# Performance work log

Hardware: AMD Instinct MI355X
Metric: run time of the kernel (lower is better)

## Reference

```python
import jax, jax.numpy as jnp
import numpy as np

K = 4096          # in_features
N = 11008         # out_features
GROUP = 128       # scale group size along K
PACK = 16
BATCH, SEQ = 2, 4096


def setup_inputs() -> dict:
    key = jax.random.key(0)
    k1, k2, k3, k4 = jax.random.split(key, 4)
    x = jax.random.normal(k1, (BATCH, SEQ, K), dtype=jnp.float16)
    # valid ternary codes in {0,1,2} encoding w = code - 1 in {-1,0,+1}
    codes = jax.random.randint(k2, (K, N), 0, 3, dtype=jnp.int32)
    codes = codes.reshape(K // PACK, PACK, N)
    shifts = (2 * jnp.arange(PACK, dtype=jnp.int32))[None, :, None]
    packed_weight = jnp.sum(codes << shifts, axis=1).astype(jnp.int32)  # (K//16, N)
    scales = (jax.random.uniform(k3, (K // GROUP, N), dtype=jnp.float32) * 0.1 + 0.01).astype(jnp.float16)
    bias = (jax.random.normal(k4, (N,), dtype=jnp.float32) * 0.01).astype(jnp.float16)
    return {"x": x, "packed_weight": packed_weight, "scales": scales, "bias": bias}


def _dequant(packed_weight, scales):
    # unpack 16 two-bit codes per int32 along K
    shifts = (2 * jnp.arange(PACK, dtype=jnp.int32))[None, :, None]
    codes = (packed_weight[:, None, :] >> shifts) & 3        # (K//16, 16, N)
    Kp = packed_weight.shape[0] * PACK
    Nn = packed_weight.shape[1]
    w = (codes.astype(jnp.float16) - jnp.float16(1.0)).reshape(Kp, Nn)  # ternary {-1,0,1}
    scale_full = jnp.repeat(scales, GROUP, axis=0)            # (K, N) group-wise gamma
    return w * scale_full


def reference(x, packed_weight, scales, bias):
    Kp = packed_weight.shape[0] * PACK
    Nn = packed_weight.shape[1]
    w = _dequant(packed_weight, scales)                       # (K, N) fp16
    x2 = x.reshape(-1, Kp).astype(jnp.float16)                # (M, K)
    out = jnp.dot(x2, w, preferred_element_type=jnp.float32).astype(jnp.float16)
    out = out + bias
    return out.reshape(*x.shape[:-1], Nn)
```

## Files before the change

kernel.cpp:

```cpp
#include <hip/hip_runtime.h>
#include <stdint.h>

#define K_DIM 4096
#define N_DIM 11008
#define M_DIM 8192
#define BM 128
#define BN 128
#define BK 32
#define ASTRIDE 32
#define BSTRIDE 40
#define NSLAB (K_DIM / BK)

typedef _Float16 half8  __attribute__((ext_vector_type(8)));
typedef _Float16 half2v __attribute__((ext_vector_type(2)));
typedef float    floatx4 __attribute__((ext_vector_type(4)));

__global__ __launch_bounds__(256, 2) void ternary_gemm(
    const float* __restrict__ x,
    const int*   __restrict__ pw,
    const float* __restrict__ scales,
    const float* __restrict__ bias,
    float*       __restrict__ out)
{
    __shared__ __align__(16) _Float16 lds_a[BM * ASTRIDE];
    __shared__ __align__(16) _Float16 lds_b[BN * BSTRIDE];

    const int tid  = threadIdx.x;
    const int lane = tid & 63;
    const int wave = tid >> 6;

    const int n0 = blockIdx.x * BN;
    const int m0 = blockIdx.y * BM;

    const int wm = (wave & 1) * 64;
    const int wn = (wave >> 1) * 64;

    const int nb  = tid & 127;
    const int kpi = tid >> 7;
    const int*   pwp = pw + (size_t)kpi * N_DIM + n0 + nb;
    const float* scp = scales + n0 + nb;
    _Float16* bl = lds_b + nb * BSTRIDE + kpi * 16;

    floatx4 acc[4][4];
    #pragma unroll
    for (int i = 0; i < 4; ++i)
        #pragma unroll
        for (int j = 0; j < 4; ++j)
            acc[i][j] = floatx4{0.f, 0.f, 0.f, 0.f};

    const int lr = lane & 15;
    const int qk = (lane >> 4) * 8;

    for (int slab = 0; slab < NSLAB; ++slab) {
        const int k0 = slab * BK;

        #pragma unroll
        for (int i = 0; i < 4; ++i) {
            const int idx = tid + i * 256;
            const int row = idx >> 3;
            const int kq  = (idx & 7) * 4;
            float4 v4 = *(const float4*)(x + (size_t)(m0 + row) * K_DIM + k0 + kq);
            half2v h0; h0[0] = (_Float16)v4.x; h0[1] = (_Float16)v4.y;
            half2v h1; h1[0] = (_Float16)v4.z; h1[1] = (_Float16)v4.w;
            *(uint2*)(lds_a + row * ASTRIDE + kq) =
                make_uint2(__builtin_bit_cast(uint32_t, h0),
                           __builtin_bit_cast(uint32_t, h1));
        }

        uint32_t v  = (uint32_t)pwp[(size_t)slab * 2 * N_DIM];
        _Float16 sh = (_Float16)scp[(size_t)(slab >> 2) * N_DIM];
        uint32_t sbits = (uint32_t)__builtin_bit_cast(unsigned short, sh);
        uint32_t tmpl = sbits | (((sbits >> 8) ^ 0x80u) << 24);

        uint32_t q[8];
        #pragma unroll
        for (int j = 0; j < 8; ++j) {
            uint32_t t4 = (v >> (4 * j)) & 0xFu;
            uint32_t sp = (t4 | (t4 << 14)) & 0x00030003u;
            uint32_t sel = ((sp & 0x00010001u) << 1) | ((0x00030003u - sp) << 8);
            q[j] = __builtin_amdgcn_perm(tmpl, tmpl, sel);
        }
        *(uint4*)(bl)     = make_uint4(q[0], q[1], q[2], q[3]);
        *(uint4*)(bl + 8) = make_uint4(q[4], q[5], q[6], q[7]);

        __syncthreads();

        half8 af[4], bfr[4];
        #pragma unroll
        for (int t = 0; t < 4; ++t) {
            af[t]  = *(const half8*)&lds_a[(wm + t * 16 + lr) * ASTRIDE + qk];
            bfr[t] = *(const half8*)&lds_b[(wn + t * 16 + lr) * BSTRIDE + qk];
        }
        #pragma unroll
        for (int mt = 0; mt < 4; ++mt)
            #pragma unroll
            for (int nt = 0; nt < 4; ++nt)
                acc[mt][nt] = __builtin_amdgcn_mfma_f32_16x16x32_f16(
                    af[mt], bfr[nt], acc[mt][nt], 0, 0, 0);

        __syncthreads();
    }

    float bv[4];
    #pragma unroll
    for (int nt = 0; nt < 4; ++nt) bv[nt] = bias[n0 + wn + nt * 16 + lr];

    const int rbase = (lane >> 4) * 4;
    #pragma unroll
    for (int mt = 0; mt < 4; ++mt) {
        #pragma unroll
        for (int nt = 0; nt < 4; ++nt) {
            const int col = n0 + wn + nt * 16 + lr;
            float* op = out + (size_t)(m0 + wm + mt * 16 + rbase) * N_DIM + col;
            floatx4 a = acc[mt][nt];
            #pragma unroll
            for (int r = 0; r < 4; ++r)
                op[(size_t)r * N_DIM] = a[r] + bv[nt];
        }
    }
}

extern "C" void kernel_launch(void* const* d_in, const int* in_sizes, int n_in,
                              void* d_out, int out_size, void* d_ws, size_t ws_size,
                              hipStream_t stream) {
    const float* x  = (const float*)d_in[0];
    const int*   pw = (const int*)d_in[1];
    const float* sc = (const float*)d_in[2];
    const float* bs = (const float*)d_in[3];
    float* out = (float*)d_out;

    dim3 grid(N_DIM / BN, M_DIM / BM);
    ternary_gemm<<<grid, 256, 0, stream>>>(x, pw, sc, bs, out);
}
```

Measured before the change: 1.263 ms.

## Split into x conversion, weight dequant prepass, and async-LDS fp16 GEMM

```diff
diff --git a/kernel.cpp b/kernel.cpp
--- a/kernel.cpp
+++ b/kernel.cpp
@@ -7,23 +7,68 @@
 #define BM 128
 #define BN 128
 #define BK 32
-#define ASTRIDE 32
-#define BSTRIDE 40
 #define NSLAB (K_DIM / BK)
 
-typedef _Float16 half8  __attribute__((ext_vector_type(8)));
-typedef _Float16 half2v __attribute__((ext_vector_type(2)));
+typedef _Float16 half8   __attribute__((ext_vector_type(8)));
+typedef _Float16 half2v  __attribute__((ext_vector_type(2)));
 typedef float    floatx4 __attribute__((ext_vector_type(4)));
 
-__global__ __launch_bounds__(256, 2) void ternary_gemm(
-    const float* __restrict__ x,
-    const int*   __restrict__ pw,
-    const float* __restrict__ scales,
-    const float* __restrict__ bias,
-    float*       __restrict__ out)
-{
-    __shared__ __align__(16) _Float16 lds_a[BM * ASTRIDE];
-    __shared__ __align__(16) _Float16 lds_b[BN * BSTRIDE];
+#define WS_X16_BYTES  ((size_t)M_DIM * K_DIM * 2)
+#define WS_W16_BYTES  ((size_t)N_DIM * K_DIM * 2)
+#define WS_NEEDED     (WS_X16_BYTES + WS_W16_BYTES)
+
+__device__ __forceinline__ void async_load16(const void* g, void* l) {
+    __builtin_amdgcn_global_load_lds(
+        (const __attribute__((address_space(1))) void*)g,
+        (__attribute__((address_space(3))) void*)l,
+        16, 0, 0);
+}
+
+__global__ __launch_bounds__(256) void convert_x(
+    const float* __restrict__ x, _Float16* __restrict__ x16)
+{
+    const size_t i = ((size_t)blockIdx.x * 256 + threadIdx.x) * 8;
+    float4 a = *(const float4*)(x + i);
+    float4 b = *(const float4*)(x + i + 4);
+    half8 h;
+    h[0] = (_Float16)a.x; h[1] = (_Float16)a.y; h[2] = (_Float16)a.z; h[3] = (_Float16)a.w;
+    h[4] = (_Float16)b.x; h[5] = (_Float16)b.y; h[6] = (_Float16)b.z; h[7] = (_Float16)b.w;
+    *(half8*)(x16 + i) = h;
+}
+
+__global__ __launch_bounds__(256) void dequant_w(
+    const int* __restrict__ pw, const float* __restrict__ scales,
+    _Float16* __restrict__ w16t)
+{
+    const int kp = (int)(blockIdx.x * 16) + (int)(threadIdx.x & 15);
+    const int n  = (int)(blockIdx.y * 16) + (int)(threadIdx.x >> 4);
+
+    uint32_t v  = (uint32_t)pw[(size_t)kp * N_DIM + n];
+    _Float16 sh = (_Float16)scales[(size_t)(kp >> 3) * N_DIM + n];
+    uint32_t sbits = (uint32_t)__builtin_bit_cast(unsigned short, sh);
+    uint32_t tmpl  = sbits | (((sbits >> 8) ^ 0x80u) << 24);
+
+    uint32_t q[8];
+    #pragma unroll
+    for (int j = 0; j < 8; ++j) {
+        uint32_t t4 = (v >> (4 * j)) & 0xFu;
+        uint32_t sp = (t4 | (t4 << 14)) & 0x00030003u;
+        uint32_t sel = ((sp & 0x00010001u) << 1) | ((0x00030003u - sp) << 8);
+        q[j] = __builtin_amdgcn_perm(tmpl, tmpl, sel);
+    }
+    _Float16* dst = w16t + (size_t)n * K_DIM + (size_t)kp * 16;
+    *(uint4*)(dst)     = make_uint4(q[0], q[1], q[2], q[3]);
+    *(uint4*)(dst + 8) = make_uint4(q[4], q[5], q[6], q[7]);
+}
+
+__global__ __launch_bounds__(256, 2) void gemm_f16(
+    const _Float16* __restrict__ x16,
+    const _Float16* __restrict__ w16t,
+    const float*    __restrict__ bias,
+    float*          __restrict__ out)
+{
+    __shared__ __align__(16) _Float16 lds_a[BM * BK];
+    __shared__ __align__(16) _Float16 lds_b[BN * BK];
 
     const int tid  = threadIdx.x;
     const int lane = tid & 63;
@@ -32,6 +77,87 @@
     const int n0 = blockIdx.x * BN;
     const int m0 = blockIdx.y * BM;
 
+    const int wm = (wave & 1) * 64;
+    const int wn = (wave >> 1) * 64;
+
+    const int sr = tid >> 2;
+    const int sk = (tid & 3) * 8;
+    const _Float16* ag0 = x16  + (size_t)(m0 + sr) * K_DIM + sk;
+    const _Float16* ag1 = ag0 + (size_t)64 * K_DIM;
+    const _Float16* bg0 = w16t + (size_t)(n0 + sr) * K_DIM + sk;
+    const _Float16* bg1 = bg0 + (size_t)64 * K_DIM;
+    _Float16* al = lds_a + tid * 8;
+    _Float16* blp = lds_b + tid * 8;
+
+    floatx4 acc[4][4];
+    #pragma unroll
+    for (int i = 0; i < 4; ++i)
+        #pragma unroll
+        for (int j = 0; j < 4; ++j)
+            acc[i][j] = floatx4{0.f, 0.f, 0.f, 0.f};
+
+    const int lr = lane & 15;
+    const int qk = (lane >> 4) * 8;
+
+    for (int slab = 0; slab < NSLAB; ++slab) {
+        const size_t ko = (size_t)slab * BK;
+        async_load16(ag0 + ko, al);
+        async_load16(ag1 + ko, al + 2048);
+        async_load16(bg0 + ko, blp);
+        async_load16(bg1 + ko, blp + 2048);
+
+        __syncthreads();
+
+        half8 af[4], bf[4];
+        #pragma unroll
+        for (int t = 0; t < 4; ++t) {
+            af[t] = *(const half8*)&lds_a[(wm + t * 16 + lr) * BK + qk];
+            bf[t] = *(const half8*)&lds_b[(wn + t * 16 + lr) * BK + qk];
+        }
+        #pragma unroll
+        for (int mt = 0; mt < 4; ++mt)
+            #pragma unroll
+            for (int nt = 0; nt < 4; ++nt)
+                acc[mt][nt] = __builtin_amdgcn_mfma_f32_16x16x32_f16(
+                    af[mt], bf[nt], acc[mt][nt], 0, 0, 0);
+
+        __syncthreads();
+    }
+
+    float bv[4];
+    #pragma unroll
+    for (int nt = 0; nt < 4; ++nt) bv[nt] = bias[n0 + wn + nt * 16 + lr];
+
+    const int rbase = (lane >> 4) * 4;
+    #pragma unroll
+    for (int mt = 0; mt < 4; ++mt) {
+        #pragma unroll
+        for (int nt = 0; nt < 4; ++nt) {
+            const int col = n0 + wn + nt * 16 + lr;
+            float* op = out + (size_t)(m0 + wm + mt * 16 + rbase) * N_DIM + col;
+            floatx4 a = acc[mt][nt];
+            #pragma unroll
+            for (int r = 0; r < 4; ++r)
+                op[(size_t)r * N_DIM] = a[r] + bv[nt];
+        }
+    }
+}
+
+#define ASTRIDE 40
+#define BSTRIDE 40
+__global__ __launch_bounds__(256, 2) void ternary_gemm_fused(
+    const float* __restrict__ x, const int* __restrict__ pw,
+    const float* __restrict__ scales, const float* __restrict__ bias,
+    float* __restrict__ out)
+{
+    __shared__ __align__(16) _Float16 lds_a[BM * ASTRIDE];
+    __shared__ __align__(16) _Float16 lds_b[BN * BSTRIDE];
+
+    const int tid  = threadIdx.x;
+    const int lane = tid & 63;
+    const int wave = tid >> 6;
+    const int n0 = blockIdx.x * BN;
+    const int m0 = blockIdx.y * BM;
     const int wm = (wave & 1) * 64;
     const int wn = (wave >> 1) * 64;
 
@@ -53,7 +179,6 @@
 
     for (int slab = 0; slab < NSLAB; ++slab) {
         const int k0 = slab * BK;
-
         #pragma unroll
         for (int i = 0; i < 4; ++i) {
             const int idx = tid + i * 256;
@@ -66,12 +191,10 @@
                 make_uint2(__builtin_bit_cast(uint32_t, h0),
                            __builtin_bit_cast(uint32_t, h1));
         }
-
         uint32_t v  = (uint32_t)pwp[(size_t)slab * 2 * N_DIM];
         _Float16 sh = (_Float16)scp[(size_t)(slab >> 2) * N_DIM];
         uint32_t sbits = (uint32_t)__builtin_bit_cast(unsigned short, sh);
         uint32_t tmpl = sbits | (((sbits >> 8) ^ 0x80u) << 24);
-
         uint32_t q[8];
         #pragma unroll
         for (int j = 0; j < 8; ++j) {
@@ -104,7 +227,6 @@
     float bv[4];
     #pragma unroll
     for (int nt = 0; nt < 4; ++nt) bv[nt] = bias[n0 + wn + nt * 16 + lr];
-
     const int rbase = (lane >> 4) * 4;
     #pragma unroll
     for (int mt = 0; mt < 4; ++mt) {
@@ -130,5 +252,15 @@
     float* out = (float*)d_out;
 
     dim3 grid(N_DIM / BN, M_DIM / BM);
-    ternary_gemm<<<grid, 256, 0, stream>>>(x, pw, sc, bs, out);
-}
+
+    if (ws_size >= WS_NEEDED) {
+        _Float16* x16  = (_Float16*)d_ws;
+        _Float16* w16t = (_Float16*)((char*)d_ws + WS_X16_BYTES);
+        convert_x<<<(M_DIM * (size_t)K_DIM) / (8 * 256), 256, 0, stream>>>(x, x16);
+        dim3 dq_grid((K_DIM / 16) / 16, N_DIM / 16);
+        dequant_w<<<dq_grid, 256, 0, stream>>>(pw, sc, w16t);
+        gemm_f16<<<grid, 256, 0, stream>>>(x16, w16t, bs, out);
+    } else {
+        ternary_gemm_fused<<<grid, 256, 0, stream>>>(x, pw, sc, bs, out);
+    }
+}
```

Result: slower. 1.681 ms (+33.1%).
